# Optimization experiments

Measured on AMD Instinct MI355X. Metric: run time of the kernel, lower is better.

## Reference

```python
import jax, jax.numpy as jnp
import numpy as np

B, L, LTXT = 4, 1024, 128
D_MODEL, TEXT_DIM = 768, 768
D_INNER, D_STATE, D_CONV, DT_RANK = 2 * D_MODEL, 16, 4, (D_MODEL + 15) // 16


def setup_inputs() -> dict:
    key = jax.random.key(0)
    ks = jax.random.split(key, 10)
    s = 0.02
    f32 = jnp.float32
    # A_log init as in mamba_ssm: A = repeat(arange(1, d_state+1))
    A_log = jnp.log(jnp.broadcast_to(jnp.arange(1, D_STATE + 1, dtype=f32), (D_INNER, D_STATE)))
    return {
        "image_tokens": jax.random.normal(ks[0], (B, L, D_MODEL), f32),
        "text_tokens": jax.random.normal(ks[1], (B, LTXT, TEXT_DIM), f32),
        "W_txt": s * jax.random.normal(ks[2], (D_MODEL, TEXT_DIM), f32),
        "b_txt": jnp.zeros((D_MODEL,), f32),
        "in_proj_w": s * jax.random.normal(ks[3], (2 * D_INNER, D_MODEL), f32),
        "conv_w": s * jax.random.normal(ks[4], (D_INNER, 1, D_CONV), f32),
        "conv_b": jnp.zeros((D_INNER,), f32),
        "x_proj_w": s * jax.random.normal(ks[5], (DT_RANK + 2 * D_STATE, D_INNER), f32),
        "dt_proj_w": s * jax.random.normal(ks[6], (D_INNER, DT_RANK), f32),
        "dt_proj_b": jnp.full((D_INNER,), -4.6, f32),  # inv-softplus of small dt init
        "A_log": A_log,
        "D": jnp.ones((D_INNER,), f32),
        "out_proj_w": s * jax.random.normal(ks[7], (D_MODEL, D_INNER), f32),
    }


def _mamba(tokens, in_proj_w, conv_w, conv_b, x_proj_w, dt_proj_w, dt_proj_b, A_log, D, out_proj_w):
    Bsz = tokens.shape[0]
    # input projection -> x, z each (B, L, d_inner)
    xz = tokens @ in_proj_w.T
    x, z = jnp.split(xz, 2, axis=-1)
    # causal depthwise conv1d over L + SiLU
    x_bdl = jnp.transpose(x, (0, 2, 1))  # (B, d_inner, L)
    x_conv = jax.lax.conv_general_dilated(
        x_bdl, conv_w, (1,), [(D_CONV - 1, 0)],
        dimension_numbers=("NCH", "OIH", "NCH"), feature_group_count=D_INNER,
    ) + conv_b[None, :, None]
    x = jax.nn.silu(jnp.transpose(x_conv, (0, 2, 1)))  # (B, L, d_inner)
    # input-dependent SSM params
    x_dbl = x @ x_proj_w.T  # (B, L, dt_rank + 2*d_state)
    dt_r = x_dbl[..., :DT_RANK]
    Bm = x_dbl[..., DT_RANK:DT_RANK + D_STATE]  # (B, L, d_state)
    Cm = x_dbl[..., DT_RANK + D_STATE:]         # (B, L, d_state)
    dt = jax.nn.softplus(dt_r @ dt_proj_w.T + dt_proj_b)  # (B, L, d_inner)
    A = -jnp.exp(A_log)  # (d_inner, d_state)

    def step(h, inp):
        dt_t, B_t, C_t, u_t = inp  # (B,d_inner),(B,d_state),(B,d_state),(B,d_inner)
        dA = jnp.exp(dt_t[:, :, None] * A)                  # (B, d_inner, d_state)
        h = dA * h + (dt_t * u_t)[:, :, None] * B_t[:, None, :]
        y = jnp.einsum("bds,bs->bd", h, C_t)
        return h, y

    h0 = jnp.zeros((Bsz, D_INNER, D_STATE), tokens.dtype)
    xs = (
        jnp.transpose(dt, (1, 0, 2)),
        jnp.transpose(Bm, (1, 0, 2)),
        jnp.transpose(Cm, (1, 0, 2)),
        jnp.transpose(x, (1, 0, 2)),
    )
    _, ys = jax.lax.scan(step, h0, xs)  # ys: (L, B, d_inner)
    y = jnp.transpose(ys, (1, 0, 2)) + x * D
    y = y * jax.nn.silu(z)
    return y @ out_proj_w.T  # (B, L, d_model)


def reference(image_tokens, text_tokens, W_txt, b_txt, in_proj_w, conv_w, conv_b,
              x_proj_w, dt_proj_w, dt_proj_b, A_log, D, out_proj_w):
    # text_pool='cls' -> take token 0
    txt = text_tokens[:, 0, :] @ W_txt.T + b_txt          # (B, d_model)
    tokens = image_tokens + txt[:, None, :]                # broadcast add
    y = _mamba(tokens, in_proj_w, conv_w, conv_b, x_proj_w,
               dt_proj_w, dt_proj_b, A_log, D, out_proj_w)
    # AdaptiveAvgPool1d(1) over sequence dim, then squeeze -> (B, d_model)
    return y.mean(axis=1)
```

## Files before the change

### kernel.cpp

```cpp
#include <hip/hip_runtime.h>
#include <math.h>

constexpr int kB   = 4;
constexpr int kL   = 1024;
constexpr int kDM  = 768;
constexpr int kDI  = 1536;
constexpr int kDS  = 16;
constexpr int kDTR = 48;
constexpr int kNX  = 80;
constexpr int kM   = kB * kL;
constexpr int kLTXT = 128;

typedef __attribute__((ext_vector_type(8))) short bf16x8;
typedef __attribute__((ext_vector_type(4))) float f32x4;

__device__ inline unsigned short f2bf(float f) {
    unsigned u = __float_as_uint(f);
    u = (u + 0x7FFFu + ((u >> 16) & 1u)) >> 16;
    return (unsigned short)u;
}

__device__ __forceinline__ void gl2lds16(const unsigned short* g, unsigned short* l) {
    __builtin_amdgcn_global_load_lds(
        (const __attribute__((address_space(1))) unsigned int*)g,
        (__attribute__((address_space(3))) unsigned int*)l, 16, 0, 0);
}

__global__ __launch_bounds__(256) void txt_kernel(
    const float* __restrict__ text, const float* __restrict__ Wt,
    const float* __restrict__ bt, float* __restrict__ txt)
{
    int gw = blockIdx.x * 4 + (threadIdx.x >> 6);
    int lane = threadIdx.x & 63;
    int b = gw / kDM;
    int j = gw - b * kDM;
    const float* trow = text + (size_t)b * kLTXT * kDM;
    const float* wrow = Wt + (size_t)j * kDM;
    float acc = 0.f;
    for (int k = lane; k < kDM; k += 64) acc = fmaf(trow[k], wrow[k], acc);
    #pragma unroll
    for (int o = 32; o; o >>= 1) acc += __shfl_xor(acc, o, 64);
    if (lane == 0) txt[gw] = acc + bt[j];
}

__global__ __launch_bounds__(256) void tokens_bf16_kernel(
    const float* __restrict__ img, const float* __restrict__ txt,
    unsigned short* __restrict__ tok)
{
    int i = blockIdx.x * 256 + threadIdx.x;
    float4 a = ((const float4*)img)[i];
    int m = i / (kDM / 4);
    int k4 = i - m * (kDM / 4);
    float4 tv = ((const float4*)(txt + (size_t)(m >> 10) * kDM))[k4];
    ushort4 o;
    o.x = f2bf(a.x + tv.x); o.y = f2bf(a.y + tv.y);
    o.z = f2bf(a.z + tv.z); o.w = f2bf(a.w + tv.w);
    ((ushort4*)tok)[i] = o;
}

__global__ __launch_bounds__(256) void castw_kernel(
    const float* __restrict__ w, unsigned short* __restrict__ o, int n4)
{
    int i = blockIdx.x * 256 + threadIdx.x;
    if (i >= n4) return;
    float4 a = ((const float4*)w)[i];
    ushort4 v;
    v.x = f2bf(a.x); v.y = f2bf(a.y); v.z = f2bf(a.z); v.w = f2bf(a.w);
    ((ushort4*)o)[i] = v;
}

__global__ __launch_bounds__(256) void mfma_inproj_kernel(
    const unsigned short* __restrict__ A, const unsigned short* __restrict__ W,
    float* __restrict__ xout, float* __restrict__ gout)
{
    __shared__ unsigned short Asm[2][128][32];
    __shared__ unsigned short Wsm[2][128][32];
    const int t = threadIdx.x;
    const int lane = t & 63;
    const int wv = t >> 6;
    const int wr = wv >> 1, wc = wv & 1;
    const int m0 = blockIdx.x * 128;
    const int n0 = blockIdx.y * 128;

    const int srow = lane >> 2;
    const int scol = (lane & 3) * 8;
    const unsigned short* agp  = A + (size_t)(m0 + wv * 32 + srow) * kDM + scol;
    const unsigned short* agp2 = agp + 16 * kDM;
    const unsigned short* wgp  = W + (size_t)(n0 + wv * 32 + srow) * kDM + scol;
    const unsigned short* wgp2 = wgp + 16 * kDM;

    auto stage = [&](int buf, int k0) {
        gl2lds16(agp  + k0, &Asm[buf][wv * 32][0]);
        gl2lds16(agp2 + k0, &Asm[buf][wv * 32 + 16][0]);
        gl2lds16(wgp  + k0, &Wsm[buf][wv * 32][0]);
        gl2lds16(wgp2 + k0, &Wsm[buf][wv * 32 + 16][0]);
    };

    f32x4 acc[4][4] = {};
    const int fr = lane & 15;
    const int fk = (lane >> 4) * 8;

    stage(0, 0);
    __syncthreads();

    int buf = 0;
    for (int k0 = 0; k0 < kDM; k0 += 32) {
        if (k0 + 32 < kDM) stage(buf ^ 1, k0 + 32);
        bf16x8 af[4], wf[4];
        #pragma unroll
        for (int i = 0; i < 4; ++i)
            af[i] = *(const bf16x8*)&Asm[buf][wr * 64 + i * 16 + fr][fk];
        #pragma unroll
        for (int j = 0; j < 4; ++j)
            wf[j] = *(const bf16x8*)&Wsm[buf][wc * 64 + j * 16 + fr][fk];
        #pragma unroll
        for (int i = 0; i < 4; ++i)
            #pragma unroll
            for (int j = 0; j < 4; ++j)
                acc[i][j] = __builtin_amdgcn_mfma_f32_16x16x32_bf16(af[i], wf[j], acc[i][j], 0, 0, 0);
        __syncthreads();
        buf ^= 1;
    }

    const int erow = (lane >> 4) * 4;
    const int ecol = lane & 15;
    #pragma unroll
    for (int i = 0; i < 4; ++i) {
        #pragma unroll
        for (int j = 0; j < 4; ++j) {
            const int gn = n0 + wc * 64 + j * 16 + ecol;
            #pragma unroll
            for (int q = 0; q < 4; ++q) {
                const int gm = m0 + wr * 64 + i * 16 + erow + q;
                float v = acc[i][j][q];
                if (gn < kDI) {
                    xout[(size_t)gm * kDI + gn] = v;
                } else {
                    gout[(size_t)gm * kDI + (gn - kDI)] = v / (1.f + __expf(-v));
                }
            }
        }
    }
}

constexpr int kKS   = 8;
constexpr int kKSEG = kDI / kKS;

__global__ __launch_bounds__(256) void xproj_splitk_kernel(
    const float* __restrict__ A, const float* __restrict__ W,
    float* __restrict__ part)
{
    __shared__ float As[16][68];
    __shared__ float Ws[16][84];
    const int t = threadIdx.x;
    const int m0 = blockIdx.x * 64;
    const int kbase = blockIdx.y * kKSEG;
    const int lrow = t >> 2, lk4 = (t & 3) << 2;
    const int ci = (t & 15) << 2;
    const int cj = (t >> 4) * 5;
    float acc[4][5] = {};
    const float* aptr = A + (size_t)(m0 + lrow) * kDI + kbase + lk4;

    for (int k0 = 0; k0 < kKSEG; k0 += 16) {
        float4 av = *(const float4*)(aptr + k0);
        if (k0) __syncthreads();
        As[lk4+0][lrow] = av.x; As[lk4+1][lrow] = av.y;
        As[lk4+2][lrow] = av.z; As[lk4+3][lrow] = av.w;
        #pragma unroll
        for (int i = 0; i < 5; ++i) {
            int idx = t + 256 * i;
            int n = idx % 80;
            int k = idx / 80;
            Ws[k][n] = W[(size_t)n * kDI + kbase + k0 + k];
        }
        __syncthreads();
        #pragma unroll
        for (int k = 0; k < 16; ++k) {
            const float4 a4 = *(const float4*)&As[k][ci];
            const float aa[4] = {a4.x, a4.y, a4.z, a4.w};
            float ww[5];
            #pragma unroll
            for (int j = 0; j < 5; ++j) ww[j] = Ws[k][cj + j];
            #pragma unroll
            for (int i = 0; i < 4; ++i)
                #pragma unroll
                for (int j = 0; j < 5; ++j)
                    acc[i][j] = fmaf(aa[i], ww[j], acc[i][j]);
        }
    }

    float* pbase = part + ((size_t)blockIdx.y * kM) * kNX;
    #pragma unroll
    for (int i = 0; i < 4; ++i)
        #pragma unroll
        for (int j = 0; j < 5; ++j)
            pbase[(size_t)(m0 + ci + i) * kNX + cj + j] = acc[i][j];
}

__global__ __launch_bounds__(256) void xproj_reduce_kernel(
    const float* __restrict__ part, float* __restrict__ xdbl)
{
    int i = blockIdx.x * 256 + threadIdx.x;
    float s = 0.f;
    #pragma unroll
    for (int k = 0; k < kKS; ++k) s += part[(size_t)k * kM * kNX + i];
    xdbl[i] = s;
}

__global__ __launch_bounds__(256) void conv_silu_kernel(
    const float* __restrict__ xraw, const float* __restrict__ cw,
    const float* __restrict__ cb, float* __restrict__ xout)
{
    int i = blockIdx.x * 256 + threadIdx.x;
    int d4 = i % (kDI / 4);
    int ml = i / (kDI / 4);
    int l = ml & (kL - 1);
    const int d = d4 * 4;
    float4 acc = *(const float4*)&cb[d];
    const float* base = xraw + (size_t)ml * kDI + d - 3 * (size_t)kDI;
    float4 w0 = *(const float4*)&cw[(d + 0) * 4];
    float4 w1 = *(const float4*)&cw[(d + 1) * 4];
    float4 w2 = *(const float4*)&cw[(d + 2) * 4];
    float4 w3 = *(const float4*)&cw[(d + 3) * 4];
    const float wj[4][4] = {{w0.x, w1.x, w2.x, w3.x}, {w0.y, w1.y, w2.y, w3.y},
                            {w0.z, w1.z, w2.z, w3.z}, {w0.w, w1.w, w2.w, w3.w}};
    #pragma unroll
    for (int j = 0; j < 4; ++j) {
        if (l - 3 + j >= 0) {
            float4 xv = *(const float4*)(base + (size_t)j * kDI);
            acc.x = fmaf(xv.x, wj[j][0], acc.x);
            acc.y = fmaf(xv.y, wj[j][1], acc.y);
            acc.z = fmaf(xv.z, wj[j][2], acc.z);
            acc.w = fmaf(xv.w, wj[j][3], acc.w);
        }
    }
    acc.x /= (1.f + __expf(-acc.x));
    acc.y /= (1.f + __expf(-acc.y));
    acc.z /= (1.f + __expf(-acc.z));
    acc.w /= (1.f + __expf(-acc.w));
    *(float4*)&xout[(size_t)ml * kDI + d] = acc;
}

constexpr int kNSEG = 16;
constexpr int kSEGL = kL / kNSEG;
constexpr int kXP   = 84;
constexpr int kP    = kB * kDI * 16;

__global__ __launch_bounds__(256) void scan5_kernel(
    const float* __restrict__ x, const float* __restrict__ g,
    const float* __restrict__ xdbl, const float* __restrict__ Wd,
    const float* __restrict__ dt_bias, const float* __restrict__ A_log,
    float* __restrict__ PA, float* __restrict__ QA,
    float* __restrict__ accA, float* __restrict__ wcA,
    float* __restrict__ ugA)
{
    __shared__ float xdS[kSEGL][kXP];
    __shared__ float uS [kSEGL][16];
    __shared__ float gS [kSEGL][16];
    __shared__ float dtS[kSEGL][17];
    const int t = threadIdx.x;
    const int blk = blockIdx.x;
    const int seg = blk & (kNSEG - 1);
    const int bd  = blk >> 4;
    const int b   = bd / 96;
    const int d0  = (bd % 96) * 16;
    const int lb  = seg * kSEGL;

    const int sl = t >> 2, sc = (t & 3) << 2;
    const float* x_base  = x  + ((size_t)b << 10) * kDI + d0;
    const float* g_base  = g  + ((size_t)b << 10) * kDI + d0;
    const float* xd_base = xdbl + ((size_t)b << 10) * kNX;

    *(float4*)&uS[sl][sc] = *(const float4*)(x_base + (size_t)(lb + sl) * kDI + sc);
    *(float4*)&gS[sl][sc] = *(const float4*)(g_base + (size_t)(lb + sl) * kDI + sc);
    #pragma unroll
    for (int j = 0; j < 5; ++j) {
        int idx = t + 256 * j;
        int row = idx / 20, col4 = idx % 20;
        *(float4*)&xdS[row][col4 * 4] =
            *(const float4*)(xd_base + (size_t)(lb + row) * kNX + col4 * 4);
    }

    const int s = t & 15;
    const int c = t >> 4;
    const int d = d0 + c;
    const float Aval = -__expf(A_log[d * kDS + s]);

    const int cc = t & 15, ii = t >> 4;
    float4 wreg[12];
    {
        const float* wrow = Wd + (size_t)(d0 + cc) * kDTR;
        #pragma unroll
        for (int i = 0; i < 12; ++i) wreg[i] = *(const float4*)(wrow + i * 4);
    }
    const float bn = dt_bias[d0 + cc];

    __syncthreads();

    #pragma unroll
    for (int q = 0; q < 4; ++q) {
        const int i = ii * 4 + q;
        float a = bn;
        #pragma unroll
        for (int k4 = 0; k4 < 12; ++k4) {
            const float4 xv = *(const float4*)&xdS[i][k4 * 4];
            a = fmaf(xv.x, wreg[k4].x, a);
            a = fmaf(xv.y, wreg[k4].y, a);
            a = fmaf(xv.z, wreg[k4].z, a);
            a = fmaf(xv.w, wreg[k4].w, a);
        }
        a = (a > 20.f) ? a : log1pf(__expf(a));
        dtS[i][cc] = a;
    }
    __syncthreads();

    float h = 0.f, cp = 1.f, acc = 0.f, wc = 0.f, ug = 0.f;
    #pragma unroll 8
    for (int i = 0; i < kSEGL; ++i) {
        const float dtv = dtS[i][c];
        const float uv  = uS [i][c];
        const float gv  = gS [i][c];
        const float Bv  = xdS[i][kDTR + s];
        const float Cv  = xdS[i][kDTR + 16 + s];
        const float dA  = __expf(dtv * Aval);
        h  = fmaf(dA, h, dtv * uv * Bv);
        cp = cp * dA;
        const float cg = Cv * gv;
        acc = fmaf(h, cg, acc);
        wc  = fmaf(cp, cg, wc);
        ug  = fmaf(uv, gv, ug);
    }

    const int p = (((b * kDI + d) << 4) | s);
    const size_t o = (size_t)seg * kP + p;
    PA[o] = cp; QA[o] = h; accA[o] = acc; wcA[o] = wc;
    if (s == 0) ugA[(size_t)seg * (kB * kDI) + b * kDI + d] = ug;
}

__global__ __launch_bounds__(256) void scan_combine_kernel(
    const float* __restrict__ PA, const float* __restrict__ QA,
    const float* __restrict__ accA, const float* __restrict__ wcA,
    const float* __restrict__ ugA, const float* __restrict__ Dvec,
    float* __restrict__ ysum)
{
    const int p = blockIdx.x * 256 + threadIdx.x;
    const int s = p & 15;
    const int bd = p >> 4;
    float h = 0.f, tot = 0.f;
    #pragma unroll
    for (int seg = 0; seg < kNSEG; ++seg) {
        const size_t o = (size_t)seg * kP + p;
        tot += accA[o] + h * wcA[o];
        h = fmaf(PA[o], h, QA[o]);
    }
    #pragma unroll
    for (int o2 = 1; o2 < 16; o2 <<= 1) tot += __shfl_xor(tot, o2, 64);
    if (s == 0) {
        float ug = 0.f;
        #pragma unroll
        for (int seg = 0; seg < kNSEG; ++seg)
            ug += ugA[(size_t)seg * (kB * kDI) + bd];
        ysum[bd] = tot + Dvec[bd % kDI] * ug;
    }
}

__global__ __launch_bounds__(256) void final_kernel(
    const float* __restrict__ ysum, const float* __restrict__ Wout,
    float* __restrict__ out)
{
    int gw = blockIdx.x * 4 + (threadIdx.x >> 6);
    int lane = threadIdx.x & 63;
    int b = gw / kDM;
    int j = gw - b * kDM;
    const float* yrow = ysum + (size_t)b * kDI;
    const float* wrow = Wout + (size_t)j * kDI;
    float acc = 0.f;
    for (int k = lane; k < kDI; k += 64) acc = fmaf(yrow[k], wrow[k], acc);
    #pragma unroll
    for (int o = 32; o; o >>= 1) acc += __shfl_xor(acc, o, 64);
    if (lane == 0) out[gw] = acc * (1.f / (float)kL);
}

extern "C" void kernel_launch(void* const* d_in, const int* in_sizes, int n_in,
                              void* d_out, int out_size, void* d_ws, size_t ws_size,
                              hipStream_t stream)
{
    const float* image_tokens = (const float*)d_in[0];
    const float* text_tokens  = (const float*)d_in[1];
    const float* W_txt        = (const float*)d_in[2];
    const float* b_txt        = (const float*)d_in[3];
    const float* in_proj_w    = (const float*)d_in[4];
    const float* conv_w       = (const float*)d_in[5];
    const float* conv_b       = (const float*)d_in[6];
    const float* x_proj_w     = (const float*)d_in[7];
    const float* dt_proj_w    = (const float*)d_in[8];
    const float* dt_proj_b    = (const float*)d_in[9];
    const float* A_log        = (const float*)d_in[10];
    const float* Dvec         = (const float*)d_in[11];
    const float* out_proj_w   = (const float*)d_in[12];
    float* out = (float*)d_out;

    char* p = (char*)d_ws;
    float* txt = (float*)p;                       p += 12288;
    unsigned short* tokb = (unsigned short*)p;    p += (size_t)kM * kDM * 2;
    unsigned short* wb   = (unsigned short*)p;    p += (size_t)2 * kDI * kDM * 2;
    float* xraw = (float*)p;                      p += (size_t)kM * kDI * 4;
    float* gbuf = (float*)p;                      p += (size_t)kM * kDI * 4;
    float* xbuf = (float*)p;                      p += (size_t)kM * kDI * 4;
    float* xdbl = (float*)p;                      p += (size_t)kM * kNX * 4;
    float* ysum = (float*)p;                      p += (size_t)kB * kDI * 4;
    float* part = (float*)tokb;
    float* PA   = xraw;
    float* QA   = PA + (size_t)kNSEG * kP;
    float* accA = QA + (size_t)kNSEG * kP;
    float* wcA  = accA + (size_t)kNSEG * kP;
    float* ugA  = part;

    txt_kernel<<<dim3(kB * kDM / 4), dim3(256), 0, stream>>>(text_tokens, W_txt, b_txt, txt);

    tokens_bf16_kernel<<<dim3(kM * kDM / 4 / 256), dim3(256), 0, stream>>>(image_tokens, txt, tokb);

    castw_kernel<<<dim3((2 * kDI * kDM / 4 + 255) / 256), dim3(256), 0, stream>>>(
        in_proj_w, wb, 2 * kDI * kDM / 4);

    mfma_inproj_kernel<<<dim3(kM / 128, 2 * kDI / 128), dim3(256), 0, stream>>>(
        tokb, wb, xraw, gbuf);

    conv_silu_kernel<<<dim3(kM * kDI / 4 / 256), dim3(256), 0, stream>>>(
        xraw, conv_w, conv_b, xbuf);

    xproj_splitk_kernel<<<dim3(kM / 64, kKS), dim3(256), 0, stream>>>(xbuf, x_proj_w, part);
    xproj_reduce_kernel<<<dim3(kM * kNX / 256), dim3(256), 0, stream>>>(part, xdbl);

    scan5_kernel<<<dim3(kB * 96 * kNSEG), dim3(256), 0, stream>>>(
        xbuf, gbuf, xdbl, dt_proj_w, dt_proj_b, A_log,
        PA, QA, accA, wcA, ugA);
    scan_combine_kernel<<<dim3(kP / 256), dim3(256), 0, stream>>>(
        PA, QA, accA, wcA, ugA, Dvec, ysum);

    final_kernel<<<dim3(kB * kDM / 4), dim3(256), 0, stream>>>(ysum, out_proj_w, out);
}
```

Baseline: 180.1 us.

## Widen scan blocks to 32 channels with two states per thread

The segmented scan kernel now handles 32 channels per block, and each thread owns two SSM states of one channel instead of one, so the grid is halved. Each thread computes dt for its own channel once in registers and writes it back into the reused xdS buffer, which removes the separate dtS array and lets the per-step dt, u and g loads serve two states. The exponential uses exp2 with A prescaled by log2(e), and outputs are stored as float2. This trades more registers per thread (launch bounds ask for 4 blocks per unit) and an extra barrier for fewer LDS reads and less redundant dt projection work.

```diff
diff --git a/kernel.cpp b/kernel.cpp
--- a/kernel.cpp
+++ b/kernel.cpp
@@ -13,6 +13,7 @@
 
 typedef __attribute__((ext_vector_type(8))) short bf16x8;
 typedef __attribute__((ext_vector_type(4))) float f32x4;
+typedef __attribute__((ext_vector_type(2))) float f32x2;
 
 __device__ inline unsigned short f2bf(float f) {
     unsigned u = __float_as_uint(f);
@@ -243,10 +244,12 @@
 
 constexpr int kNSEG = 16;
 constexpr int kSEGL = kL / kNSEG;
+constexpr int kCH   = 32;
 constexpr int kXP   = 84;
 constexpr int kP    = kB * kDI * 16;
-
-__global__ __launch_bounds__(256) void scan5_kernel(
+constexpr float kLOG2E = 1.44269504089f;
+
+__global__ __launch_bounds__(256, 4) void scan6_kernel(
     const float* __restrict__ x, const float* __restrict__ g,
     const float* __restrict__ xdbl, const float* __restrict__ Wd,
     const float* __restrict__ dt_bias, const float* __restrict__ A_log,
@@ -255,86 +258,101 @@
     float* __restrict__ ugA)
 {
     __shared__ float xdS[kSEGL][kXP];
-    __shared__ float uS [kSEGL][16];
-    __shared__ float gS [kSEGL][16];
-    __shared__ float dtS[kSEGL][17];
+    __shared__ float uS [kSEGL][kCH];
+    __shared__ float gS [kSEGL][kCH];
     const int t = threadIdx.x;
     const int blk = blockIdx.x;
     const int seg = blk & (kNSEG - 1);
     const int bd  = blk >> 4;
-    const int b   = bd / 96;
-    const int d0  = (bd % 96) * 16;
+    const int b   = bd / 48;
+    const int d0  = (bd % 48) * kCH;
     const int lb  = seg * kSEGL;
 
-    const int sl = t >> 2, sc = (t & 3) << 2;
     const float* x_base  = x  + ((size_t)b << 10) * kDI + d0;
     const float* g_base  = g  + ((size_t)b << 10) * kDI + d0;
     const float* xd_base = xdbl + ((size_t)b << 10) * kNX;
 
-    *(float4*)&uS[sl][sc] = *(const float4*)(x_base + (size_t)(lb + sl) * kDI + sc);
-    *(float4*)&gS[sl][sc] = *(const float4*)(g_base + (size_t)(lb + sl) * kDI + sc);
+    #pragma unroll
+    for (int j = 0; j < 2; ++j) {
+        int idx = t + 256 * j;
+        int row = idx >> 3, c4 = (idx & 7) * 4;
+        *(float4*)&uS[row][c4] = *(const float4*)(x_base + (size_t)(lb + row) * kDI + c4);
+        *(float4*)&gS[row][c4] = *(const float4*)(g_base + (size_t)(lb + row) * kDI + c4);
+    }
     #pragma unroll
     for (int j = 0; j < 5; ++j) {
         int idx = t + 256 * j;
-        int row = idx / 20, col4 = idx % 20;
-        *(float4*)&xdS[row][col4 * 4] =
-            *(const float4*)(xd_base + (size_t)(lb + row) * kNX + col4 * 4);
-    }
-
-    const int s = t & 15;
-    const int c = t >> 4;
-    const int d = d0 + c;
-    const float Aval = -__expf(A_log[d * kDS + s]);
-
-    const int cc = t & 15, ii = t >> 4;
+        int row = idx / 20, c4 = idx % 20;
+        *(float4*)&xdS[row][c4 * 4] =
+            *(const float4*)(xd_base + (size_t)(lb + row) * kNX + c4 * 4);
+    }
+
+    const int c  = t & 31;
+    const int sp = t >> 5;
+    const int d  = d0 + c;
+    f32x2 Av2;
+    Av2.x = -__expf(A_log[d * kDS + 2 * sp])     * kLOG2E;
+    Av2.y = -__expf(A_log[d * kDS + 2 * sp + 1]) * kLOG2E;
+
     float4 wreg[12];
     {
-        const float* wrow = Wd + (size_t)(d0 + cc) * kDTR;
+        const float* wrow = Wd + (size_t)d * kDTR;
         #pragma unroll
         for (int i = 0; i < 12; ++i) wreg[i] = *(const float4*)(wrow + i * 4);
     }
-    const float bn = dt_bias[d0 + cc];
+    const float bn = dt_bias[d];
 
     __syncthreads();
 
-    #pragma unroll
-    for (int q = 0; q < 4; ++q) {
-        const int i = ii * 4 + q;
+    float dtv[8];
+    #pragma unroll
+    for (int q = 0; q < 8; ++q) {
+        const int r = sp * 8 + q;
         float a = bn;
         #pragma unroll
         for (int k4 = 0; k4 < 12; ++k4) {
-            const float4 xv = *(const float4*)&xdS[i][k4 * 4];
+            const float4 xv = *(const float4*)&xdS[r][k4 * 4];
             a = fmaf(xv.x, wreg[k4].x, a);
             a = fmaf(xv.y, wreg[k4].y, a);
             a = fmaf(xv.z, wreg[k4].z, a);
             a = fmaf(xv.w, wreg[k4].w, a);
         }
-        a = (a > 20.f) ? a : log1pf(__expf(a));
-        dtS[i][cc] = a;
+        dtv[q] = (a > 20.f) ? a : log1pf(__expf(a));
     }
     __syncthreads();
-
-    float h = 0.f, cp = 1.f, acc = 0.f, wc = 0.f, ug = 0.f;
+    #pragma unroll
+    for (int q = 0; q < 8; ++q) xdS[sp * 8 + q][c] = dtv[q];
+    __syncthreads();
+
+    f32x2 h = {0.f, 0.f}, cp = {1.f, 1.f}, acc = {0.f, 0.f}, wc = {0.f, 0.f};
+    float ug = 0.f;
     #pragma unroll 8
     for (int i = 0; i < kSEGL; ++i) {
-        const float dtv = dtS[i][c];
+        const float dtc = xdS[i][c];
         const float uv  = uS [i][c];
         const float gv  = gS [i][c];
-        const float Bv  = xdS[i][kDTR + s];
-        const float Cv  = xdS[i][kDTR + 16 + s];
-        const float dA  = __expf(dtv * Aval);
-        h  = fmaf(dA, h, dtv * uv * Bv);
+        const f32x2 Bv = *(const f32x2*)&xdS[i][kDTR + 2 * sp];
+        const f32x2 Cv = *(const f32x2*)&xdS[i][kDTR + 16 + 2 * sp];
+        const f32x2 pm = dtc * Av2;
+        f32x2 dA;
+        dA.x = exp2f(pm.x);
+        dA.y = exp2f(pm.y);
+        const float dtu = dtc * uv;
+        h  = dA * h + dtu * Bv;
         cp = cp * dA;
-        const float cg = Cv * gv;
-        acc = fmaf(h, cg, acc);
-        wc  = fmaf(cp, cg, wc);
+        const f32x2 cg = Cv * gv;
+        acc = h * cg + acc;
+        wc  = cp * cg + wc;
         ug  = fmaf(uv, gv, ug);
     }
 
-    const int p = (((b * kDI + d) << 4) | s);
+    const int p = ((b * kDI + d) << 4) + 2 * sp;
     const size_t o = (size_t)seg * kP + p;
-    PA[o] = cp; QA[o] = h; accA[o] = acc; wcA[o] = wc;
-    if (s == 0) ugA[(size_t)seg * (kB * kDI) + b * kDI + d] = ug;
+    *(f32x2*)&PA[o]   = cp;
+    *(f32x2*)&QA[o]   = h;
+    *(f32x2*)&accA[o] = acc;
+    *(f32x2*)&wcA[o]  = wc;
+    if (sp == 0) ugA[(size_t)seg * (kB * kDI) + b * kDI + d] = ug;
 }
 
 __global__ __launch_bounds__(256) void scan_combine_kernel(
@@ -432,7 +450,7 @@
     xproj_splitk_kernel<<<dim3(kM / 64, kKS), dim3(256), 0, stream>>>(xbuf, x_proj_w, part);
     xproj_reduce_kernel<<<dim3(kM * kNX / 256), dim3(256), 0, stream>>>(part, xdbl);
 
-    scan5_kernel<<<dim3(kB * 96 * kNSEG), dim3(256), 0, stream>>>(
+    scan6_kernel<<<dim3(kB * 48 * kNSEG), dim3(256), 0, stream>>>(
         xbuf, gbuf, xdbl, dt_proj_w, dt_proj_b, A_log,
         PA, QA, accA, wcA, ugA);
     scan_combine_kernel<<<dim3(kP / 256), dim3(256), 0, stream>>>(
```

Result: no change. 179.5 us (-0.4%).

## Split dt projection into tiled GEMM kernel and vectorize scan over states

Applied to the files above, without the earlier changes.

Moves the dt_proj matmul plus softplus out of the scan kernel into a separate LDS-tiled register-blocked GEMM that writes a full dt buffer. The scan kernel is rewritten so each thread owns four states of one channel in a float4, streams u/g/dt/B/C from global with software prefetch instead of staging through shared memory, and uses exp2 with prescaled A. The aim is to cut the recomputation of dt across state lanes and the shared-memory traffic in the scan. In exchange it adds an extra 25 MB dt write and read and one more launch, and the workspace is re-laid out to make room.

```diff
diff --git a/kernel.cpp b/kernel.cpp
--- a/kernel.cpp
+++ b/kernel.cpp
@@ -205,6 +205,60 @@
     #pragma unroll
     for (int k = 0; k < kKS; ++k) s += part[(size_t)k * kM * kNX + i];
     xdbl[i] = s;
+}
+
+__global__ __launch_bounds__(256) void dtproj3_kernel(
+    const float* __restrict__ xdbl, const float* __restrict__ Wd,
+    const float* __restrict__ bias, float* __restrict__ dt)
+{
+    __shared__ float As[48][68];
+    __shared__ float Ws[48][68];
+    const int t = threadIdx.x;
+    const int m0 = blockIdx.x * 64;
+    const int n0 = blockIdx.y * 64;
+
+    #pragma unroll
+    for (int j = 0; j < 3; ++j) {
+        int idx = t * 3 + j;
+        int row = idx / 12, c4 = (idx % 12) * 4;
+        float4 a = *(const float4*)&xdbl[(size_t)(m0 + row) * kNX + c4];
+        As[c4+0][row] = a.x; As[c4+1][row] = a.y;
+        As[c4+2][row] = a.z; As[c4+3][row] = a.w;
+        float4 w = *(const float4*)&Wd[(size_t)(n0 + row) * kDTR + c4];
+        Ws[c4+0][row] = w.x; Ws[c4+1][row] = w.y;
+        Ws[c4+2][row] = w.z; Ws[c4+3][row] = w.w;
+    }
+    __syncthreads();
+
+    const int ci = (t & 15) * 4;
+    const int cj = (t >> 4) * 4;
+    float acc[4][4] = {};
+    #pragma unroll
+    for (int k = 0; k < kDTR; ++k) {
+        const float4 a4 = *(const float4*)&As[k][ci];
+        const float4 w4 = *(const float4*)&Ws[k][cj];
+        const float aa[4] = {a4.x, a4.y, a4.z, a4.w};
+        const float ww[4] = {w4.x, w4.y, w4.z, w4.w};
+        #pragma unroll
+        for (int i = 0; i < 4; ++i)
+            #pragma unroll
+            for (int j = 0; j < 4; ++j)
+                acc[i][j] = fmaf(aa[i], ww[j], acc[i][j]);
+    }
+
+    float4 bn = *(const float4*)&bias[n0 + cj];
+    const float bb[4] = {bn.x, bn.y, bn.z, bn.w};
+    #pragma unroll
+    for (int i = 0; i < 4; ++i) {
+        float4 o;
+        float* op = (float*)&o;
+        #pragma unroll
+        for (int j = 0; j < 4; ++j) {
+            float v = acc[i][j] + bb[j];
+            op[j] = (v > 20.f) ? v : log1pf(__expf(v));
+        }
+        *(float4*)&dt[(size_t)(m0 + ci + i) * kDI + n0 + cj] = o;
+    }
 }
 
 __global__ __launch_bounds__(256) void conv_silu_kernel(
@@ -243,98 +297,82 @@
 
 constexpr int kNSEG = 16;
 constexpr int kSEGL = kL / kNSEG;
-constexpr int kXP   = 84;
 constexpr int kP    = kB * kDI * 16;
-
-__global__ __launch_bounds__(256) void scan5_kernel(
-    const float* __restrict__ x, const float* __restrict__ g,
-    const float* __restrict__ xdbl, const float* __restrict__ Wd,
-    const float* __restrict__ dt_bias, const float* __restrict__ A_log,
+constexpr float kLOG2E = 1.44269504089f;
+
+__global__ __launch_bounds__(256, 6) void scan7_kernel(
+    const float* __restrict__ u, const float* __restrict__ g,
+    const float* __restrict__ dt, const float* __restrict__ xdbl,
+    const float* __restrict__ A_log,
     float* __restrict__ PA, float* __restrict__ QA,
     float* __restrict__ accA, float* __restrict__ wcA,
     float* __restrict__ ugA)
 {
-    __shared__ float xdS[kSEGL][kXP];
-    __shared__ float uS [kSEGL][16];
-    __shared__ float gS [kSEGL][16];
-    __shared__ float dtS[kSEGL][17];
     const int t = threadIdx.x;
     const int blk = blockIdx.x;
     const int seg = blk & (kNSEG - 1);
     const int bd  = blk >> 4;
-    const int b   = bd / 96;
-    const int d0  = (bd % 96) * 16;
+    const int b   = bd / 24;
+    const int d0  = (bd % 24) * 64;
+    const int c   = t & 63;
+    const int sq  = t >> 6;
+    const int d   = d0 + c;
     const int lb  = seg * kSEGL;
 
-    const int sl = t >> 2, sc = (t & 3) << 2;
-    const float* x_base  = x  + ((size_t)b << 10) * kDI + d0;
-    const float* g_base  = g  + ((size_t)b << 10) * kDI + d0;
-    const float* xd_base = xdbl + ((size_t)b << 10) * kNX;
-
-    *(float4*)&uS[sl][sc] = *(const float4*)(x_base + (size_t)(lb + sl) * kDI + sc);
-    *(float4*)&gS[sl][sc] = *(const float4*)(g_base + (size_t)(lb + sl) * kDI + sc);
-    #pragma unroll
-    for (int j = 0; j < 5; ++j) {
-        int idx = t + 256 * j;
-        int row = idx / 20, col4 = idx % 20;
-        *(float4*)&xdS[row][col4 * 4] =
-            *(const float4*)(xd_base + (size_t)(lb + row) * kNX + col4 * 4);
-    }
-
-    const int s = t & 15;
-    const int c = t >> 4;
-    const int d = d0 + c;
-    const float Aval = -__expf(A_log[d * kDS + s]);
-
-    const int cc = t & 15, ii = t >> 4;
-    float4 wreg[12];
+    f32x4 Av;
     {
-        const float* wrow = Wd + (size_t)(d0 + cc) * kDTR;
-        #pragma unroll
-        for (int i = 0; i < 12; ++i) wreg[i] = *(const float4*)(wrow + i * 4);
-    }
-    const float bn = dt_bias[d0 + cc];
-
-    __syncthreads();
-
-    #pragma unroll
-    for (int q = 0; q < 4; ++q) {
-        const int i = ii * 4 + q;
-        float a = bn;
-        #pragma unroll
-        for (int k4 = 0; k4 < 12; ++k4) {
-            const float4 xv = *(const float4*)&xdS[i][k4 * 4];
-            a = fmaf(xv.x, wreg[k4].x, a);
-            a = fmaf(xv.y, wreg[k4].y, a);
-            a = fmaf(xv.z, wreg[k4].z, a);
-            a = fmaf(xv.w, wreg[k4].w, a);
-        }
-        a = (a > 20.f) ? a : log1pf(__expf(a));
-        dtS[i][cc] = a;
-    }
-    __syncthreads();
-
-    float h = 0.f, cp = 1.f, acc = 0.f, wc = 0.f, ug = 0.f;
-    #pragma unroll 8
+        float4 al = *(const float4*)&A_log[d * kDS + sq * 4];
+        Av.x = -__expf(al.x) * kLOG2E;
+        Av.y = -__expf(al.y) * kLOG2E;
+        Av.z = -__expf(al.z) * kLOG2E;
+        Av.w = -__expf(al.w) * kLOG2E;
+    }
+
+    const size_t base = ((size_t)b << 10) * kDI + (size_t)lb * kDI + d;
+    const float* up  = u  + base;
+    const float* gp  = g  + base;
+    const float* dtp = dt + base;
+    const float* bp  = xdbl + ((size_t)b << 10) * kNX + (size_t)lb * kNX
+                            + kDTR + sq * 4;
+
+    float nu = *up, ng = *gp, ndt = *dtp;
+    f32x4 nB = *(const f32x4*)bp, nC = *(const f32x4*)(bp + 16);
+
+    f32x4 h  = {0.f, 0.f, 0.f, 0.f};
+    f32x4 cp = {1.f, 1.f, 1.f, 1.f};
+    f32x4 acc = {0.f, 0.f, 0.f, 0.f};
+    f32x4 wc  = {0.f, 0.f, 0.f, 0.f};
+    float ug = 0.f;
+
+    #pragma unroll 4
     for (int i = 0; i < kSEGL; ++i) {
-        const float dtv = dtS[i][c];
-        const float uv  = uS [i][c];
-        const float gv  = gS [i][c];
-        const float Bv  = xdS[i][kDTR + s];
-        const float Cv  = xdS[i][kDTR + 16 + s];
-        const float dA  = __expf(dtv * Aval);
-        h  = fmaf(dA, h, dtv * uv * Bv);
+        const float dtv = ndt, uv = nu, gv = ng;
+        const f32x4 Bv = nB, Cv = nC;
+        if (i < kSEGL - 1) {
+            up += kDI; gp += kDI; dtp += kDI; bp += kNX;
+            nu = *up; ng = *gp; ndt = *dtp;
+            nB = *(const f32x4*)bp; nC = *(const f32x4*)(bp + 16);
+        }
+        const f32x4 pm = dtv * Av;
+        f32x4 dA;
+        dA.x = exp2f(pm.x); dA.y = exp2f(pm.y);
+        dA.z = exp2f(pm.z); dA.w = exp2f(pm.w);
+        const float dtu = dtv * uv;
+        h  = dA * h + dtu * Bv;
         cp = cp * dA;
-        const float cg = Cv * gv;
-        acc = fmaf(h, cg, acc);
-        wc  = fmaf(cp, cg, wc);
+        const f32x4 cg = Cv * gv;
+        acc = h * cg + acc;
+        wc  = cp * cg + wc;
         ug  = fmaf(uv, gv, ug);
     }
 
-    const int p = (((b * kDI + d) << 4) | s);
+    const int p = ((b * kDI + d) << 4) + sq * 4;
     const size_t o = (size_t)seg * kP + p;
-    PA[o] = cp; QA[o] = h; accA[o] = acc; wcA[o] = wc;
-    if (s == 0) ugA[(size_t)seg * (kB * kDI) + b * kDI + d] = ug;
+    *(f32x4*)&PA[o]   = cp;
+    *(f32x4*)&QA[o]   = h;
+    *(f32x4*)&accA[o] = acc;
+    *(f32x4*)&wcA[o]  = wc;
+    if (sq == 0) ugA[(size_t)seg * (kB * kDI) + b * kDI + d] = ug;
 }
 
 __global__ __launch_bounds__(256) void scan_combine_kernel(
@@ -401,20 +439,23 @@
     float* out = (float*)d_out;
 
     char* p = (char*)d_ws;
-    float* txt = (float*)p;                       p += 12288;
-    unsigned short* tokb = (unsigned short*)p;    p += (size_t)kM * kDM * 2;
-    unsigned short* wb   = (unsigned short*)p;    p += (size_t)2 * kDI * kDM * 2;
+    float* txt  = (float*)p;                      p += 12288;
+    float* dtreg = (float*)p;                     p += (size_t)kM * kDI * 4;
     float* xraw = (float*)p;                      p += (size_t)kM * kDI * 4;
     float* gbuf = (float*)p;                      p += (size_t)kM * kDI * 4;
     float* xbuf = (float*)p;                      p += (size_t)kM * kDI * 4;
     float* xdbl = (float*)p;                      p += (size_t)kM * kNX * 4;
-    float* ysum = (float*)p;                      p += (size_t)kB * kDI * 4;
-    float* part = (float*)tokb;
+    float* ysum = (float*)p;                      p += 32768;
+    float* ugA  = (float*)p;                      p += (size_t)kNSEG * kB * kDI * 4;
+
+    unsigned short* tokb = (unsigned short*)dtreg;
+    unsigned short* wb   = tokb + (size_t)kM * kDM;
+    float* part = dtreg;
+    float* dtb  = dtreg;
     float* PA   = xraw;
     float* QA   = PA + (size_t)kNSEG * kP;
     float* accA = QA + (size_t)kNSEG * kP;
     float* wcA  = accA + (size_t)kNSEG * kP;
-    float* ugA  = part;
 
     txt_kernel<<<dim3(kB * kDM / 4), dim3(256), 0, stream>>>(text_tokens, W_txt, b_txt, txt);
 
@@ -432,9 +473,11 @@
     xproj_splitk_kernel<<<dim3(kM / 64, kKS), dim3(256), 0, stream>>>(xbuf, x_proj_w, part);
     xproj_reduce_kernel<<<dim3(kM * kNX / 256), dim3(256), 0, stream>>>(part, xdbl);
 
-    scan5_kernel<<<dim3(kB * 96 * kNSEG), dim3(256), 0, stream>>>(
-        xbuf, gbuf, xdbl, dt_proj_w, dt_proj_b, A_log,
-        PA, QA, accA, wcA, ugA);
+    dtproj3_kernel<<<dim3(kM / 64, kDI / 64), dim3(256), 0, stream>>>(
+        xdbl, dt_proj_w, dt_proj_b, dtb);
+
+    scan7_kernel<<<dim3(kB * 24 * kNSEG), dim3(256), 0, stream>>>(
+        xbuf, gbuf, dtb, xdbl, A_log, PA, QA, accA, wcA, ugA);
     scan_combine_kernel<<<dim3(kP / 256), dim3(256), 0, stream>>>(
         PA, QA, accA, wcA, ugA, Dvec, ysum);
 
```

After: 301.7 us. 67.5% more time.
